# Kernel optimization log

Measured on AMD Instinct MI355X. Metric: run time of the kernel, lower is better.

The kernel has to match this reference:

```python
import jax, jax.numpy as jnp
import numpy as np

N = 50000  # nodes
E = 1600000  # edges
L = 2  # layers
D = 128  # input/hidden dim


def setup_inputs() -> dict:
    key = jax.random.key(0)
    ks = jax.random.split(key, 8)
    s = 1.0 / np.sqrt(D)
    return {
        "x": jax.random.normal(ks[0], (N, D), jnp.float32),
        "edge_index": jax.random.randint(ks[1], (2, E), 0, N, jnp.int64),
        "h": jax.random.normal(ks[2], (L, N, D), jnp.float32),
        "Wx": jax.random.normal(ks[3], (L, 3, D, D), jnp.float32) * s,
        "bx": jax.random.normal(ks[4], (L, 3, D), jnp.float32) * 0.01,
        "Wh": jax.random.normal(ks[5], (L, 3, D, D), jnp.float32) * s,
        "bh": jax.random.normal(ks[6], (L, 3, D), jnp.float32) * 0.01,
    }


def _gcn(x, W, b, src, dst, dinv):
    # GCNConv with added self-loops and symmetric normalization:
    # out = D^{-1/2} (A + I) D^{-1/2} X W + b
    hw = x @ W                                   # [N, H]
    norm = dinv[src] * dinv[dst]                 # [E]
    msg = hw[src] * norm[:, None]                # [E, H]
    agg = jax.ops.segment_sum(msg, dst, num_segments=N)
    agg = agg + hw * (dinv * dinv)[:, None]      # self-loop contribution
    return agg + b


def reference(x, edge_index, h, Wx, bx, Wh, bh):
    src = edge_index[0]
    dst = edge_index[1]
    # in-degree on destination nodes, including self-loop (+1)
    deg = jax.ops.segment_sum(jnp.ones((E,), x.dtype), dst, num_segments=N) + 1.0
    dinv = jax.lax.rsqrt(deg)

    outs = []
    inp = x
    for l in range(L):
        hl = h[l]
        z = jax.nn.sigmoid(_gcn(inp, Wx[l, 0], bx[l, 0], src, dst, dinv)
                           + _gcn(hl, Wh[l, 0], bh[l, 0], src, dst, dinv))
        r = jax.nn.sigmoid(_gcn(inp, Wx[l, 1], bx[l, 1], src, dst, dinv)
                           + _gcn(hl, Wh[l, 1], bh[l, 1], src, dst, dinv))
        h_tilde = jnp.tanh(_gcn(inp, Wx[l, 2], bx[l, 2], src, dst, dinv)
                           + _gcn(r * hl, Wh[l, 2], bh[l, 2], src, dst, dinv))
        out = z * hl + (1.0 - z) * h_tilde
        outs.append(out)
        inp = out
    return jnp.stack(outs, axis=0)  # [L, N, H]
```

## Files before the change

kernel.cpp:

```cpp
#include <hip/hip_runtime.h>

typedef __attribute__((ext_vector_type(8))) unsigned short us8;
typedef __attribute__((ext_vector_type(8))) short s8;
typedef __attribute__((ext_vector_type(4))) float f4;
typedef __attribute__((ext_vector_type(2))) float f2;

#define DEV static __device__ __forceinline__
#define CAP 128
#define NRG 128
#define NBB 256
#define SEGC 128

DEV float bf2f(unsigned short h){ return __uint_as_float(((unsigned)h)<<16); }
DEV unsigned short f2bf(float f){
  unsigned x = __float_as_uint(f);
  x += 0x7fffu + ((x>>16)&1u);
  return (unsigned short)(x>>16);
}
DEV float sigm(float x){ return 1.f/(1.f + __expf(-x)); }

__global__ __launch_bounds__(256) void k_bucket(const int* __restrict__ src,
    const int* __restrict__ dst, unsigned* __restrict__ buf,
    int* __restrict__ cnt2, int e, int n){
  __shared__ int lcnt[NRG];
  int b = blockIdx.x;
  for(int i=threadIdx.x;i<NRG;i+=256) lcnt[i] = 0;
  __syncthreads();
  int chunk = (e + NBB - 1)/NBB;
  int lo = b*chunk;
  int hi = lo + chunk; if(hi>e) hi=e;
  for(int i = lo + threadIdx.x; i < hi; i += 256){
    int d = dst[i], s = src[i];
    int r = (d*NRG)/n;
    int pos = atomicAdd(&lcnt[r], 1);
    if(pos < SEGC)
      buf[((size_t)r*NBB + b)*SEGC + pos] = ((unsigned)d<<16) | (unsigned)s;
  }
  __syncthreads();
  for(int i=threadIdx.x;i<NRG;i+=256) cnt2[i*NBB + b] = lcnt[i];
}

__global__ __launch_bounds__(256) void k_build2(const unsigned* __restrict__ buf,
    const int* __restrict__ cnt2, int* __restrict__ cnt,
    unsigned short* __restrict__ col, int n){
  int r = blockIdx.x;
  int lo = (r*n + NRG-1)/NRG;
  int hi = ((r+1)*n + NRG-1)/NRG;
  int span = hi - lo;
  __shared__ int lc[512];
  for(int i=threadIdx.x; i<span; i+=256) lc[i] = 0;
  __syncthreads();
  int lane = threadIdx.x & 63;
  for(int seg = threadIdx.x>>6; seg < NBB; seg += 4){
    int c = cnt2[r*NBB + seg]; if(c > SEGC) c = SEGC;
    const unsigned* p = buf + ((size_t)r*NBB + seg)*SEGC;
    for(int i = lane; i < c; i += 64){
      unsigned v = p[i];
      int d = (int)(v >> 16), s = (int)(v & 0xffffu);
      int slot = atomicAdd(&lc[d - lo], 1);
      col[(size_t)d*CAP + slot] = (unsigned short)s;
    }
  }
  __syncthreads();
  for(int i=threadIdx.x; i<span; i+=256) cnt[lo + i] = lc[i];
}

__global__ void k_setup(const int* __restrict__ cnt, float* __restrict__ dinv, int n,
                        const float* __restrict__ Wx, const float* __restrict__ Wh,
                        unsigned short* __restrict__ WT){
  int gN = (n + 255)/256;
  int b = blockIdx.x;
  if(b < gN){
    int i = b*256 + threadIdx.x;
    if(i<n) dinv[i] = rsqrtf((float)cnt[i] + 1.0f);
  } else {
    int i = (b-gN)*256 + threadIdx.x;
    int m = i >> 15;
    int rem = i & 32767;
    int j = rem >> 8;
    int k = rem & 255;
    float v = (k<128) ? Wx[((size_t)m*128 + k)*128 + j]
                      : Wh[((size_t)m*128 + (k-128))*128 + j];
    WT[(size_t)m*32768 + j*256 + k] = f2bf(v);
  }
}

__global__ void k_scale2(const float* __restrict__ inp, const float* __restrict__ hl,
                         const float* __restrict__ dinv, unsigned char* __restrict__ y2, int n){
  int i = blockIdx.x*blockDim.x+threadIdx.x;
  if(i >= n*32) return;
  int node = i>>5, d0 = (i&31)*4;
  float dv = dinv[node];
  f4 a = *(const f4*)(inp + (size_t)node*128 + d0);
  f4 b = *(const f4*)(hl  + (size_t)node*128 + d0);
  unsigned pa = __builtin_amdgcn_cvt_pk_fp8_f32(dv*a[0], dv*a[1], 0, false);
  pa = __builtin_amdgcn_cvt_pk_fp8_f32(dv*a[2], dv*a[3], pa, true);
  unsigned pb = __builtin_amdgcn_cvt_pk_fp8_f32(dv*b[0], dv*b[1], 0, false);
  pb = __builtin_amdgcn_cvt_pk_fp8_f32(dv*b[2], dv*b[3], pb, true);
  *(unsigned*)(y2 + (size_t)node*256 + d0)       = pa;
  *(unsigned*)(y2 + (size_t)node*256 + 128 + d0) = pb;
}

template<int DB>
__global__ __launch_bounds__(256) void k_agg(const unsigned char* __restrict__ y,
    const int* __restrict__ cnt, const unsigned short* __restrict__ col,
    const float* __restrict__ dinv, unsigned short* __restrict__ out0, int n)
{
  constexpr int GL = DB/16;
  constexpr int NG = 64/GL;
  constexpr int U = 8;
  int tid = threadIdx.x;
  int wave = tid>>6, lane = tid&63;
  int g = lane/GL, gl = lane%GL;
  int node = blockIdx.x*(4*NG) + wave*NG + g;
  if(node >= n) return;
  const unsigned char* yb = y + (size_t)gl*16;
  float acc[16];
  {
    uint4 q = *(const uint4*)(yb + (size_t)node*DB);
    const unsigned* qw = (const unsigned*)&q;
    #pragma unroll
    for(int w=0;w<4;++w){
      f2 lo = __builtin_amdgcn_cvt_pk_f32_fp8(qw[w], false);
      f2 hi = __builtin_amdgcn_cvt_pk_f32_fp8(qw[w], true);
      acc[w*4+0]=lo[0]; acc[w*4+1]=lo[1]; acc[w*4+2]=hi[0]; acc[w*4+3]=hi[1];
    }
  }
  const unsigned short* myrow = col + (size_t)node*CAP;
  int c_ = cnt[node];
  int last = c_ - 1;
  for(int i=0; i<c_; i += U){
    int s[U];
    #pragma unroll
    for(int u=0;u<U;++u){
      int ii = i + u; ii = (ii < last) ? ii : last;
      s[u] = myrow[ii];
    }
    uint4 v[U];
    #pragma unroll
    for(int u=0;u<U;++u) v[u] = *(const uint4*)(yb + (size_t)s[u]*DB);
    #pragma unroll
    for(int u=0;u<U;++u){
      if(i + u < c_){
        const unsigned* qw = (const unsigned*)&v[u];
        #pragma unroll
        for(int w=0;w<4;++w){
          f2 lo = __builtin_amdgcn_cvt_pk_f32_fp8(qw[w], false);
          f2 hi = __builtin_amdgcn_cvt_pk_f32_fp8(qw[w], true);
          acc[w*4+0]+=lo[0]; acc[w*4+1]+=lo[1]; acc[w*4+2]+=hi[0]; acc[w*4+3]+=hi[1];
        }
      }
    }
  }
  float dv = dinv[node];
  us8 w0, w1;
  #pragma unroll
  for(int j=0;j<8;++j){ w0[j]=f2bf(acc[j]*dv); w1[j]=f2bf(acc[8+j]*dv); }
  int c = gl*16;
  *(us8*)(out0 + (size_t)node*DB + c)     = w0;
  *(us8*)(out0 + (size_t)node*DB + c + 8) = w1;
}

template<int KB>
DEV void stageB512(unsigned char* Bs, const unsigned short* Bsrc, int srcStride,
                   int srcOff, int t){
  constexpr int CPR = KB/8;
  #pragma unroll
  for(int i=0;i<128*CPR/512;++i){
    int c = t + i*512;
    int j = c / CPR, kc = c % CPR;
    us8 v = *(const us8*)(Bsrc + (size_t)j*srcStride + srcOff + kc*8);
    *(us8*)(Bs + ((j*(KB*2) + kc*16) ^ ((j&7)<<4))) = v;
  }
}
template<int NK>
DEV void loadA(const unsigned short* A, int astride, int arow, int nrows, int hi,
               s8 (&a)[NK]){
  const unsigned short* Ap = A + (size_t)(arow < nrows ? arow : 0)*astride + hi*8;
  #pragma unroll
  for(int kk=0;kk<NK;++kk) a[kk] = *(const s8*)(Ap + kk*32);
  if(arow >= nrows){
    #pragma unroll
    for(int kk=0;kk<NK;++kk) a[kk] = (s8)(short)0;
  }
}
template<int KB, int NK, int NA>
DEV void mfmaR(const unsigned char* Bs, const s8 (&a)[NA], int lo, int hi,
               f4 (&acc)[8]){
  static_assert(NK <= NA, "not enough A fragments");
  #pragma unroll
  for(int kk=0;kk<NK;++kk){
    #pragma unroll
    for(int n=0;n<8;++n){
      int j = n*16+lo;
      s8 b = *(const s8*)(Bs + ((j*(KB*2) + kk*64 + hi*16) ^ ((lo&7)<<4)));
      acc[n] = __builtin_amdgcn_mfma_f32_16x16x32_bf16(a[kk], b, acc[n], 0,0,0);
    }
  }
}

__global__ __launch_bounds__(512) void k_gemmRH(
    const unsigned short* __restrict__ axah, const unsigned short* __restrict__ Wr,
    const unsigned short* __restrict__ Wh2, const float* __restrict__ hl,
    const float* __restrict__ dinv, const float* __restrict__ bxr,
    const float* __restrict__ bhr, unsigned char* __restrict__ yq,
    unsigned short* __restrict__ Zbh, int nrows)
{
  __shared__ unsigned char Bs[65536];
  const int t = threadIdx.x, lane = t & 63, lo = lane & 15, hi = lane >> 4;
  const int r0 = blockIdx.x*128 + (t>>6)*16;
  const int arow = r0 + lo;
  s8 a256[8];
  loadA<8>(axah, 256, arow, nrows, hi, a256);
  stageB512<256>(Bs, Wr, 256, 0, t);
  f4 acc[8];
  #pragma unroll
  for(int n=0;n<8;++n) acc[n]=(f4)0.f;
  __syncthreads();
  mfmaR<256,8,8>(Bs, a256, lo, hi, acc);
  #pragma unroll
  for(int n=0;n<8;++n){
    const int colv = n*16 + lo;
    float bz = bxr[colv] + bhr[colv];
    #pragma unroll
    for(int tt=0;tt<4;++tt){
      int row = r0 + hi*4 + tt;
      if(row < nrows){
        float r = sigm(acc[n][tt] + bz);
        float q = dinv[row] * r * hl[(size_t)row*128 + colv];
        unsigned pk = __builtin_amdgcn_cvt_pk_fp8_f32(q, q, 0, false);
        yq[(size_t)row*128 + colv] = (unsigned char)(pk & 0xff);
      }
    }
  }
  __syncthreads();
  stageB512<128>(Bs, Wh2, 256, 0, t);
  __syncthreads();
  #pragma unroll
  for(int n=0;n<8;++n) acc[n]=(f4)0.f;
  mfmaR<128,4,8>(Bs, a256, lo, hi, acc);
  #pragma unroll
  for(int n=0;n<8;++n){
    const int colv = n*16 + lo;
    #pragma unroll
    for(int tt=0;tt<4;++tt){
      int row = r0 + hi*4 + tt;
      if(row < nrows) Zbh[(size_t)row*128 + colv] = f2bf(acc[n][tt]);
    }
  }
}

__global__ __launch_bounds__(512) void k_gemmZF(
    const unsigned short* __restrict__ axah, const unsigned short* __restrict__ aq,
    const unsigned short* __restrict__ Wz, const unsigned short* __restrict__ Wh2,
    const unsigned short* __restrict__ Zbh, const float* __restrict__ hl,
    const float* __restrict__ hnext, const float* __restrict__ dinv,
    const float* __restrict__ bxz, const float* __restrict__ bhz,
    const float* __restrict__ bxh, const float* __restrict__ bhh,
    float* __restrict__ outp, unsigned char* __restrict__ y2out, int nrows)
{
  __shared__ unsigned char Bs[65536];
  const int t = threadIdx.x, lane = t & 63, lo = lane & 15, hi = lane >> 4;
  const int r0 = blockIdx.x*128 + (t>>6)*16;
  const int arow = r0 + lo;
  s8 a256[8], a128[4];
  loadA<8>(axah, 256, arow, nrows, hi, a256);
  loadA<4>(aq, 128, arow, nrows, hi, a128);
  stageB512<256>(Bs, Wz, 256, 0, t);
  f4 accZ[8], accH[8];
  #pragma unroll
  for(int n=0;n<8;++n){ accZ[n]=(f4)0.f; accH[n]=(f4)0.f; }
  __syncthreads();
  mfmaR<256,8,8>(Bs, a256, lo, hi, accZ);
  __syncthreads();
  stageB512<128>(Bs, Wh2, 256, 128, t);
  __syncthreads();
  mfmaR<128,4,4>(Bs, a128, lo, hi, accH);
  #pragma unroll
  for(int n=0;n<8;++n){
    const int colv = n*16 + lo;
    float bz = bxz[colv] + bhz[colv];
    float bh = bxh[colv] + bhh[colv];
    #pragma unroll
    for(int tt=0;tt<4;++tt){
      int row = r0 + hi*4 + tt;
      if(row >= nrows) continue;
      float z  = sigm(accZ[n][tt] + bz);
      float ht = tanhf(accH[n][tt] + bf2f(Zbh[(size_t)row*128 + colv]) + bh);
      float ov = z*hl[(size_t)row*128 + colv] + (1.f - z)*ht;
      outp[(size_t)row*128 + colv] = ov;
      if(y2out){
        float dv = dinv[row];
        unsigned pk = __builtin_amdgcn_cvt_pk_fp8_f32(dv*ov, dv*ov, 0, false);
        y2out[(size_t)row*256 + colv] = (unsigned char)(pk & 0xff);
        float hv = dv * hnext[(size_t)row*128 + colv];
        unsigned ph = __builtin_amdgcn_cvt_pk_fp8_f32(hv, hv, 0, false);
        y2out[(size_t)row*256 + 128 + colv] = (unsigned char)(ph & 0xff);
      }
    }
  }
}

extern "C" void kernel_launch(void* const* d_in, const int* in_sizes, int n_in,
                              void* d_out, int out_size, void* d_ws, size_t ws_size,
                              hipStream_t stream){
  const float* x  = (const float*)d_in[0];
  const int*   ei = (const int*)d_in[1];
  const float* h  = (const float*)d_in[2];
  const float* Wx = (const float*)d_in[3];
  const float* bx = (const float*)d_in[4];
  const float* Wh = (const float*)d_in[5];
  const float* bh = (const float*)d_in[6];
  float* out = (float*)d_out;

  const int N = in_sizes[0] / 128;
  const int E = in_sizes[1] / 2;
  const int L = in_sizes[2] / in_sizes[0];
  const int* src = ei;
  const int* dst = ei + E;

  char* w = (char*)d_ws;
  auto alloc = [&](size_t b)->char*{ char* p = w; w += (b + 255) & ~(size_t)255; return p; };
  int* cnt = (int*)alloc((size_t)N*sizeof(int));
  unsigned short* col = (unsigned short*)alloc((size_t)N*CAP*sizeof(short));
  float* dinv = (float*)alloc((size_t)N*sizeof(float));
  unsigned short* WT = (unsigned short*)alloc((size_t)6*32768*sizeof(short));
  unsigned char* y2 = (unsigned char*)alloc((size_t)N*256);
  unsigned short* axah = (unsigned short*)alloc((size_t)N*256*sizeof(short));
  unsigned char* yq = (unsigned char*)alloc((size_t)N*128);
  unsigned short* aq = (unsigned short*)alloc((size_t)N*128*sizeof(short));
  unsigned short* Zbh = (unsigned short*)alloc((size_t)N*128*sizeof(short));
  unsigned* ebuf = (unsigned*)alloc((size_t)NRG*NBB*SEGC*sizeof(unsigned));
  int* cnt2 = (int*)alloc((size_t)NRG*NBB*sizeof(int));

  const int gN = (N + 255)/256;
  const int gew = (N*32 + 255)/256;
  const int g128 = (N + 127)/128;
  const int gagg4 = (N + 15)/16;
  const int gagg2 = (N + 31)/32;

  k_bucket<<<NBB,256,0,stream>>>(src, dst, ebuf, cnt2, E, N);
  k_build2<<<NRG,256,0,stream>>>(ebuf, cnt2, cnt, col, N);
  k_setup<<<gN + 768,256,0,stream>>>(cnt, dinv, N, Wx, Wh, WT);

  for(int l=0; l<L; ++l){
    const float* hl  = h + (size_t)l*N*128;
    const float* bxz = bx + (size_t)(l*3+0)*128; const float* bhz = bh + (size_t)(l*3+0)*128;
    const float* bxr = bx + (size_t)(l*3+1)*128; const float* bhr = bh + (size_t)(l*3+1)*128;
    const float* bxh = bx + (size_t)(l*3+2)*128; const float* bhh = bh + (size_t)(l*3+2)*128;
    const unsigned short* Wz = WT + (size_t)(l*3+0)*32768;
    const unsigned short* Wr = WT + (size_t)(l*3+1)*32768;
    const unsigned short* Wh2= WT + (size_t)(l*3+2)*32768;

    if(l==0) k_scale2<<<gew,256,0,stream>>>(x, hl, dinv, y2, N);
    k_agg<256><<<gagg4,256,0,stream>>>(y2, cnt, col, dinv, axah, N);
    k_gemmRH<<<g128,512,0,stream>>>(axah, Wr, Wh2, hl, dinv, bxr, bhr, yq, Zbh, N);
    k_agg<128><<<gagg2,256,0,stream>>>(yq, cnt, col, dinv, aq, N);
    k_gemmZF<<<g128,512,0,stream>>>(axah, aq, Wz, Wh2, Zbh, hl,
        (l+1<L) ? (h + (size_t)(l+1)*N*128) : nullptr, dinv,
        bxz, bhz, bxh, bhh, out + (size_t)l*N*128,
        (l+1<L) ? y2 : nullptr, N);
  }
}
```

Measured before the change: 370.6 us.

## Pre-convert hidden state to bf16 and widen gemmZF to 1024 threads

Converts all h layers to bf16 once inside the setup kernel and reads the bf16 copy in scale, gemmRH and gemmZF instead of fp32. gemmZF is restructured to 1024 threads, with both weight tiles staged into separate LDS buffers up front and each wave pair splitting the output columns, removing intermediate barriers. The extra conversion pass adds traffic and lowers the precision of h used in the gating blend.

```diff
diff --git a/kernel.cpp b/kernel.cpp
--- a/kernel.cpp
+++ b/kernel.cpp
@@ -1,6 +1,7 @@
 #include <hip/hip_runtime.h>
 
 typedef __attribute__((ext_vector_type(8))) unsigned short us8;
+typedef __attribute__((ext_vector_type(4))) unsigned short us4;
 typedef __attribute__((ext_vector_type(8))) short s8;
 typedef __attribute__((ext_vector_type(4))) float f4;
 typedef __attribute__((ext_vector_type(2))) float f2;
@@ -67,13 +68,15 @@
 
 __global__ void k_setup(const int* __restrict__ cnt, float* __restrict__ dinv, int n,
                         const float* __restrict__ Wx, const float* __restrict__ Wh,
-                        unsigned short* __restrict__ WT){
+                        unsigned short* __restrict__ WT,
+                        const float* __restrict__ h, unsigned short* __restrict__ hb,
+                        int htotal){
   int gN = (n + 255)/256;
   int b = blockIdx.x;
   if(b < gN){
     int i = b*256 + threadIdx.x;
     if(i<n) dinv[i] = rsqrtf((float)cnt[i] + 1.0f);
-  } else {
+  } else if(b < gN + 768){
     int i = (b-gN)*256 + threadIdx.x;
     int m = i >> 15;
     int rem = i & 32767;
@@ -82,21 +85,30 @@
     float v = (k<128) ? Wx[((size_t)m*128 + k)*128 + j]
                       : Wh[((size_t)m*128 + (k-128))*128 + j];
     WT[(size_t)m*32768 + j*256 + k] = f2bf(v);
-  }
-}
-
-__global__ void k_scale2(const float* __restrict__ inp, const float* __restrict__ hl,
+  } else {
+    size_t i = ((size_t)(b - gN - 768)*256 + threadIdx.x)*4;
+    if(i < (size_t)htotal){
+      f4 v = *(const f4*)(h + i);
+      us4 w;
+      #pragma unroll
+      for(int j=0;j<4;++j) w[j] = f2bf(v[j]);
+      *(us4*)(hb + i) = w;
+    }
+  }
+}
+
+__global__ void k_scale2(const float* __restrict__ inp, const unsigned short* __restrict__ hb0,
                          const float* __restrict__ dinv, unsigned char* __restrict__ y2, int n){
   int i = blockIdx.x*blockDim.x+threadIdx.x;
   if(i >= n*32) return;
   int node = i>>5, d0 = (i&31)*4;
   float dv = dinv[node];
   f4 a = *(const f4*)(inp + (size_t)node*128 + d0);
-  f4 b = *(const f4*)(hl  + (size_t)node*128 + d0);
+  us4 hv = *(const us4*)(hb0 + (size_t)node*128 + d0);
   unsigned pa = __builtin_amdgcn_cvt_pk_fp8_f32(dv*a[0], dv*a[1], 0, false);
   pa = __builtin_amdgcn_cvt_pk_fp8_f32(dv*a[2], dv*a[3], pa, true);
-  unsigned pb = __builtin_amdgcn_cvt_pk_fp8_f32(dv*b[0], dv*b[1], 0, false);
-  pb = __builtin_amdgcn_cvt_pk_fp8_f32(dv*b[2], dv*b[3], pb, true);
+  unsigned pb = __builtin_amdgcn_cvt_pk_fp8_f32(dv*bf2f(hv[0]), dv*bf2f(hv[1]), 0, false);
+  pb = __builtin_amdgcn_cvt_pk_fp8_f32(dv*bf2f(hv[2]), dv*bf2f(hv[3]), pb, true);
   *(unsigned*)(y2 + (size_t)node*256 + d0)       = pa;
   *(unsigned*)(y2 + (size_t)node*256 + 128 + d0) = pb;
 }
@@ -162,14 +174,13 @@
 }
 
 template<int KB>
-DEV void stageB512(unsigned char* Bs, const unsigned short* Bsrc, int srcStride,
-                   int srcOff, int t){
+DEV void stageB512(unsigned char* Bs, const unsigned short* Bsrc, int srcOff, int t){
   constexpr int CPR = KB/8;
   #pragma unroll
   for(int i=0;i<128*CPR/512;++i){
     int c = t + i*512;
     int j = c / CPR, kc = c % CPR;
-    us8 v = *(const us8*)(Bsrc + (size_t)j*srcStride + srcOff + kc*8);
+    us8 v = *(const us8*)(Bsrc + (size_t)j*256 + srcOff + kc*8);
     *(us8*)(Bs + ((j*(KB*2) + kc*16) ^ ((j&7)<<4))) = v;
   }
 }
@@ -201,7 +212,7 @@
 
 __global__ __launch_bounds__(512) void k_gemmRH(
     const unsigned short* __restrict__ axah, const unsigned short* __restrict__ Wr,
-    const unsigned short* __restrict__ Wh2, const float* __restrict__ hl,
+    const unsigned short* __restrict__ Wh2, const unsigned short* __restrict__ hbl,
     const float* __restrict__ dinv, const float* __restrict__ bxr,
     const float* __restrict__ bhr, unsigned char* __restrict__ yq,
     unsigned short* __restrict__ Zbh, int nrows)
@@ -212,7 +223,7 @@
   const int arow = r0 + lo;
   s8 a256[8];
   loadA<8>(axah, 256, arow, nrows, hi, a256);
-  stageB512<256>(Bs, Wr, 256, 0, t);
+  stageB512<256>(Bs, Wr, 0, t);
   f4 acc[8];
   #pragma unroll
   for(int n=0;n<8;++n) acc[n]=(f4)0.f;
@@ -227,14 +238,14 @@
       int row = r0 + hi*4 + tt;
       if(row < nrows){
         float r = sigm(acc[n][tt] + bz);
-        float q = dinv[row] * r * hl[(size_t)row*128 + colv];
+        float q = dinv[row] * r * bf2f(hbl[(size_t)row*128 + colv]);
         unsigned pk = __builtin_amdgcn_cvt_pk_fp8_f32(q, q, 0, false);
         yq[(size_t)row*128 + colv] = (unsigned char)(pk & 0xff);
       }
     }
   }
   __syncthreads();
-  stageB512<128>(Bs, Wh2, 256, 0, t);
+  stageB512<128>(Bs, Wh2, 0, t);
   __syncthreads();
   #pragma unroll
   for(int n=0;n<8;++n) acc[n]=(f4)0.f;
@@ -250,35 +261,80 @@
   }
 }
 
-__global__ __launch_bounds__(512) void k_gemmZF(
+DEV void stageB1k(unsigned char* Bs1, const unsigned short* W, int t){
+  #pragma unroll
+  for(int i=0;i<4;++i){
+    int c = t + i*1024;
+    int j = c >> 5, kc = c & 31;
+    us8 v = *(const us8*)(W + (size_t)j*256 + kc*8);
+    *(us8*)(Bs1 + ((j*512 + kc*16) ^ ((j&7)<<4))) = v;
+  }
+}
+DEV void stageB2k(unsigned char* Bs2, const unsigned short* W, int srcOff, int t){
+  #pragma unroll
+  for(int i=0;i<2;++i){
+    int c = t + i*1024;
+    int j = c >> 4, kc = c & 15;
+    us8 v = *(const us8*)(W + (size_t)j*256 + srcOff + kc*8);
+    *(us8*)(Bs2 + ((j*256 + kc*16) ^ ((j&7)<<4))) = v;
+  }
+}
+DEV void loadA4(const unsigned short* A, int astride, int arow, int nrows, int hi,
+                int koff, s8 (&a)[4]){
+  const unsigned short* Ap = A + (size_t)(arow < nrows ? arow : 0)*astride + koff + hi*8;
+  #pragma unroll
+  for(int kk=0;kk<4;++kk) a[kk] = *(const s8*)(Ap + kk*32);
+  if(arow >= nrows){
+    #pragma unroll
+    for(int kk=0;kk<4;++kk) a[kk] = (s8)(short)0;
+  }
+}
+template<int KROW>
+DEV void mfma4(const unsigned char* Bs, const s8 (&a)[4], int kk0, int jbase,
+               int lo, int hi, f4 (&acc)[4]){
+  #pragma unroll
+  for(int kk=0;kk<4;++kk){
+    #pragma unroll
+    for(int n=0;n<4;++n){
+      int j = jbase + n*16 + lo;
+      s8 b = *(const s8*)(Bs + ((j*KROW + (kk0+kk)*64 + hi*16) ^ ((lo&7)<<4)));
+      acc[n] = __builtin_amdgcn_mfma_f32_16x16x32_bf16(a[kk], b, acc[n], 0,0,0);
+    }
+  }
+}
+
+__global__ __launch_bounds__(1024) void k_gemmZF(
     const unsigned short* __restrict__ axah, const unsigned short* __restrict__ aq,
     const unsigned short* __restrict__ Wz, const unsigned short* __restrict__ Wh2,
-    const unsigned short* __restrict__ Zbh, const float* __restrict__ hl,
-    const float* __restrict__ hnext, const float* __restrict__ dinv,
+    const unsigned short* __restrict__ Zbh, const unsigned short* __restrict__ hbl,
+    const unsigned short* __restrict__ hbn, const float* __restrict__ dinv,
     const float* __restrict__ bxz, const float* __restrict__ bhz,
     const float* __restrict__ bxh, const float* __restrict__ bhh,
     float* __restrict__ outp, unsigned char* __restrict__ y2out, int nrows)
 {
-  __shared__ unsigned char Bs[65536];
+  __shared__ unsigned char Bs1[65536];
+  __shared__ unsigned char Bs2[32768];
   const int t = threadIdx.x, lane = t & 63, lo = lane & 15, hi = lane >> 4;
-  const int r0 = blockIdx.x*128 + (t>>6)*16;
+  const int wid = t >> 6, wrow = wid >> 1, whalf = wid & 1;
+  const int jbase = whalf*64;
+  const int r0 = blockIdx.x*128 + wrow*16;
   const int arow = r0 + lo;
-  s8 a256[8], a128[4];
-  loadA<8>(axah, 256, arow, nrows, hi, a256);
-  loadA<4>(aq, 128, arow, nrows, hi, a128);
-  stageB512<256>(Bs, Wz, 256, 0, t);
-  f4 accZ[8], accH[8];
-  #pragma unroll
-  for(int n=0;n<8;++n){ accZ[n]=(f4)0.f; accH[n]=(f4)0.f; }
-  __syncthreads();
-  mfmaR<256,8,8>(Bs, a256, lo, hi, accZ);
-  __syncthreads();
-  stageB512<128>(Bs, Wh2, 256, 128, t);
-  __syncthreads();
-  mfmaR<128,4,4>(Bs, a128, lo, hi, accH);
-  #pragma unroll
-  for(int n=0;n<8;++n){
-    const int colv = n*16 + lo;
+  stageB1k(Bs1, Wz, t);
+  stageB2k(Bs2, Wh2, 128, t);
+  s8 a03[4], a47[4], aq4[4];
+  loadA4(axah, 256, arow, nrows, hi, 0, a03);
+  loadA4(axah, 256, arow, nrows, hi, 128, a47);
+  loadA4(aq, 128, arow, nrows, hi, 0, aq4);
+  f4 accZ[4], accH[4];
+  #pragma unroll
+  for(int n=0;n<4;++n){ accZ[n]=(f4)0.f; accH[n]=(f4)0.f; }
+  __syncthreads();
+  mfma4<512>(Bs1, a03, 0, jbase, lo, hi, accZ);
+  mfma4<512>(Bs1, a47, 4, jbase, lo, hi, accZ);
+  mfma4<256>(Bs2, aq4, 0, jbase, lo, hi, accH);
+  #pragma unroll
+  for(int n=0;n<4;++n){
+    const int colv = jbase + n*16 + lo;
     float bz = bxz[colv] + bhz[colv];
     float bh = bxh[colv] + bhh[colv];
     #pragma unroll
@@ -287,13 +343,13 @@
       if(row >= nrows) continue;
       float z  = sigm(accZ[n][tt] + bz);
       float ht = tanhf(accH[n][tt] + bf2f(Zbh[(size_t)row*128 + colv]) + bh);
-      float ov = z*hl[(size_t)row*128 + colv] + (1.f - z)*ht;
+      float ov = z*bf2f(hbl[(size_t)row*128 + colv]) + (1.f - z)*ht;
       outp[(size_t)row*128 + colv] = ov;
       if(y2out){
         float dv = dinv[row];
         unsigned pk = __builtin_amdgcn_cvt_pk_fp8_f32(dv*ov, dv*ov, 0, false);
         y2out[(size_t)row*256 + colv] = (unsigned char)(pk & 0xff);
-        float hv = dv * hnext[(size_t)row*128 + colv];
+        float hv = dv * bf2f(hbn[(size_t)row*128 + colv]);
         unsigned ph = __builtin_amdgcn_cvt_pk_fp8_f32(hv, hv, 0, false);
         y2out[(size_t)row*256 + 128 + colv] = (unsigned char)(ph & 0xff);
       }
@@ -325,6 +381,7 @@
   unsigned short* col = (unsigned short*)alloc((size_t)N*CAP*sizeof(short));
   float* dinv = (float*)alloc((size_t)N*sizeof(float));
   unsigned short* WT = (unsigned short*)alloc((size_t)6*32768*sizeof(short));
+  unsigned short* hb = (unsigned short*)alloc((size_t)L*N*128*sizeof(short));
   unsigned char* y2 = (unsigned char*)alloc((size_t)N*256);
   unsigned short* axah = (unsigned short*)alloc((size_t)N*256*sizeof(short));
   unsigned char* yq = (unsigned char*)alloc((size_t)N*128);
@@ -338,13 +395,15 @@
   const int g128 = (N + 127)/128;
   const int gagg4 = (N + 15)/16;
   const int gagg2 = (N + 31)/32;
+  const int htotal = L*N*128;
+  const int ghb = (htotal + 1023)/1024;
 
   k_bucket<<<NBB,256,0,stream>>>(src, dst, ebuf, cnt2, E, N);
   k_build2<<<NRG,256,0,stream>>>(ebuf, cnt2, cnt, col, N);
-  k_setup<<<gN + 768,256,0,stream>>>(cnt, dinv, N, Wx, Wh, WT);
+  k_setup<<<gN + 768 + ghb,256,0,stream>>>(cnt, dinv, N, Wx, Wh, WT, h, hb, htotal);
 
   for(int l=0; l<L; ++l){
-    const float* hl  = h + (size_t)l*N*128;
+    const unsigned short* hbl = hb + (size_t)l*N*128;
     const float* bxz = bx + (size_t)(l*3+0)*128; const float* bhz = bh + (size_t)(l*3+0)*128;
     const float* bxr = bx + (size_t)(l*3+1)*128; const float* bhr = bh + (size_t)(l*3+1)*128;
     const float* bxh = bx + (size_t)(l*3+2)*128; const float* bhh = bh + (size_t)(l*3+2)*128;
@@ -352,12 +411,12 @@
     const unsigned short* Wr = WT + (size_t)(l*3+1)*32768;
     const unsigned short* Wh2= WT + (size_t)(l*3+2)*32768;
 
-    if(l==0) k_scale2<<<gew,256,0,stream>>>(x, hl, dinv, y2, N);
+    if(l==0) k_scale2<<<gew,256,0,stream>>>(x, hbl, dinv, y2, N);
     k_agg<256><<<gagg4,256,0,stream>>>(y2, cnt, col, dinv, axah, N);
-    k_gemmRH<<<g128,512,0,stream>>>(axah, Wr, Wh2, hl, dinv, bxr, bhr, yq, Zbh, N);
+    k_gemmRH<<<g128,512,0,stream>>>(axah, Wr, Wh2, hbl, dinv, bxr, bhr, yq, Zbh, N);
     k_agg<128><<<gagg2,256,0,stream>>>(yq, cnt, col, dinv, aq, N);
-    k_gemmZF<<<g128,512,0,stream>>>(axah, aq, Wz, Wh2, Zbh, hl,
-        (l+1<L) ? (h + (size_t)(l+1)*N*128) : nullptr, dinv,
+    k_gemmZF<<<g128,1024,0,stream>>>(axah, aq, Wz, Wh2, Zbh, hbl,
+        (l+1<L) ? (hb + (size_t)(l+1)*N*128) : nullptr, dinv,
         bxz, bhz, bxh, bhh, out + (size_t)l*N*128,
         (l+1<L) ? y2 : nullptr, N);
   }
```

New measurement: 399.9 us. 1.08x slower.

## Swap MFMA operands for row-contiguous epilogue stores and pre-convert h to bf16

Applied to the files above, without the earlier changes.

The GEMM kernels now put the weights in the MFMA A slot and node features in the B slot, so each lane owns one node and four consecutive output columns. This turns the scattered byte- and short-wide epilogue stores into vectorized 4-element stores and loads. Separately, h is converted once to bf16 in the setup kernel, halving the bytes read from h in later kernels. The cost is an extra pass over all of h in setup, and using bf16 h in the output blend instead of fp32 lowers precision.

```diff
diff --git a/kernel.cpp b/kernel.cpp
--- a/kernel.cpp
+++ b/kernel.cpp
@@ -1,6 +1,7 @@
 #include <hip/hip_runtime.h>
 
 typedef __attribute__((ext_vector_type(8))) unsigned short us8;
+typedef __attribute__((ext_vector_type(4))) unsigned short us4;
 typedef __attribute__((ext_vector_type(8))) short s8;
 typedef __attribute__((ext_vector_type(4))) float f4;
 typedef __attribute__((ext_vector_type(2))) float f2;
@@ -67,13 +68,15 @@
 
 __global__ void k_setup(const int* __restrict__ cnt, float* __restrict__ dinv, int n,
                         const float* __restrict__ Wx, const float* __restrict__ Wh,
-                        unsigned short* __restrict__ WT){
+                        unsigned short* __restrict__ WT,
+                        const float* __restrict__ h, unsigned short* __restrict__ hb,
+                        int htotal){
   int gN = (n + 255)/256;
   int b = blockIdx.x;
   if(b < gN){
     int i = b*256 + threadIdx.x;
     if(i<n) dinv[i] = rsqrtf((float)cnt[i] + 1.0f);
-  } else {
+  } else if(b < gN + 768){
     int i = (b-gN)*256 + threadIdx.x;
     int m = i >> 15;
     int rem = i & 32767;
@@ -82,21 +85,30 @@
     float v = (k<128) ? Wx[((size_t)m*128 + k)*128 + j]
                       : Wh[((size_t)m*128 + (k-128))*128 + j];
     WT[(size_t)m*32768 + j*256 + k] = f2bf(v);
-  }
-}
-
-__global__ void k_scale2(const float* __restrict__ inp, const float* __restrict__ hl,
+  } else {
+    size_t i = ((size_t)(b - gN - 768)*256 + threadIdx.x)*4;
+    if(i < (size_t)htotal){
+      f4 v = *(const f4*)(h + i);
+      us4 w;
+      #pragma unroll
+      for(int j=0;j<4;++j) w[j] = f2bf(v[j]);
+      *(us4*)(hb + i) = w;
+    }
+  }
+}
+
+__global__ void k_scale2(const float* __restrict__ inp, const unsigned short* __restrict__ hb0,
                          const float* __restrict__ dinv, unsigned char* __restrict__ y2, int n){
   int i = blockIdx.x*blockDim.x+threadIdx.x;
   if(i >= n*32) return;
   int node = i>>5, d0 = (i&31)*4;
   float dv = dinv[node];
   f4 a = *(const f4*)(inp + (size_t)node*128 + d0);
-  f4 b = *(const f4*)(hl  + (size_t)node*128 + d0);
+  us4 hv = *(const us4*)(hb0 + (size_t)node*128 + d0);
   unsigned pa = __builtin_amdgcn_cvt_pk_fp8_f32(dv*a[0], dv*a[1], 0, false);
   pa = __builtin_amdgcn_cvt_pk_fp8_f32(dv*a[2], dv*a[3], pa, true);
-  unsigned pb = __builtin_amdgcn_cvt_pk_fp8_f32(dv*b[0], dv*b[1], 0, false);
-  pb = __builtin_amdgcn_cvt_pk_fp8_f32(dv*b[2], dv*b[3], pb, true);
+  unsigned pb = __builtin_amdgcn_cvt_pk_fp8_f32(dv*bf2f(hv[0]), dv*bf2f(hv[1]), 0, false);
+  pb = __builtin_amdgcn_cvt_pk_fp8_f32(dv*bf2f(hv[2]), dv*bf2f(hv[3]), pb, true);
   *(unsigned*)(y2 + (size_t)node*256 + d0)       = pa;
   *(unsigned*)(y2 + (size_t)node*256 + 128 + d0) = pb;
 }
@@ -162,90 +174,91 @@
 }
 
 template<int KB>
-DEV void stageB512(unsigned char* Bs, const unsigned short* Bsrc, int srcStride,
-                   int srcOff, int t){
+DEV void stageB512(unsigned char* Bs, const unsigned short* Bsrc, int srcOff, int t){
   constexpr int CPR = KB/8;
   #pragma unroll
   for(int i=0;i<128*CPR/512;++i){
     int c = t + i*512;
     int j = c / CPR, kc = c % CPR;
-    us8 v = *(const us8*)(Bsrc + (size_t)j*srcStride + srcOff + kc*8);
+    us8 v = *(const us8*)(Bsrc + (size_t)j*256 + srcOff + kc*8);
     *(us8*)(Bs + ((j*(KB*2) + kc*16) ^ ((j&7)<<4))) = v;
   }
 }
 template<int NK>
-DEV void loadA(const unsigned short* A, int astride, int arow, int nrows, int hi,
-               s8 (&a)[NK]){
-  const unsigned short* Ap = A + (size_t)(arow < nrows ? arow : 0)*astride + hi*8;
-  #pragma unroll
-  for(int kk=0;kk<NK;++kk) a[kk] = *(const s8*)(Ap + kk*32);
-  if(arow >= nrows){
-    #pragma unroll
-    for(int kk=0;kk<NK;++kk) a[kk] = (s8)(short)0;
-  }
+DEV void loadB(const unsigned short* A, int astride, int node, int nrows, int hi,
+               s8 (&b)[NK]){
+  const unsigned short* Ap = A + (size_t)(node < nrows ? node : 0)*astride + hi*8;
+  #pragma unroll
+  for(int kk=0;kk<NK;++kk) b[kk] = *(const s8*)(Ap + kk*32);
 }
 template<int KB, int NK, int NA>
-DEV void mfmaR(const unsigned char* Bs, const s8 (&a)[NA], int lo, int hi,
+DEV void mfmaW(const unsigned char* Bs, const s8 (&b)[NA], int lo, int hi,
                f4 (&acc)[8]){
-  static_assert(NK <= NA, "not enough A fragments");
+  static_assert(NK <= NA, "not enough B fragments");
   #pragma unroll
   for(int kk=0;kk<NK;++kk){
     #pragma unroll
     for(int n=0;n<8;++n){
       int j = n*16+lo;
-      s8 b = *(const s8*)(Bs + ((j*(KB*2) + kk*64 + hi*16) ^ ((lo&7)<<4)));
-      acc[n] = __builtin_amdgcn_mfma_f32_16x16x32_bf16(a[kk], b, acc[n], 0,0,0);
+      s8 a = *(const s8*)(Bs + ((j*(KB*2) + kk*64 + hi*16) ^ ((lo&7)<<4)));
+      acc[n] = __builtin_amdgcn_mfma_f32_16x16x32_bf16(a, b[kk], acc[n], 0,0,0);
     }
   }
 }
 
 __global__ __launch_bounds__(512) void k_gemmRH(
     const unsigned short* __restrict__ axah, const unsigned short* __restrict__ Wr,
-    const unsigned short* __restrict__ Wh2, const float* __restrict__ hl,
+    const unsigned short* __restrict__ Wh2, const unsigned short* __restrict__ hbl,
     const float* __restrict__ dinv, const float* __restrict__ bxr,
     const float* __restrict__ bhr, unsigned char* __restrict__ yq,
     unsigned short* __restrict__ Zbh, int nrows)
 {
   __shared__ unsigned char Bs[65536];
   const int t = threadIdx.x, lane = t & 63, lo = lane & 15, hi = lane >> 4;
-  const int r0 = blockIdx.x*128 + (t>>6)*16;
-  const int arow = r0 + lo;
-  s8 a256[8];
-  loadA<8>(axah, 256, arow, nrows, hi, a256);
-  stageB512<256>(Bs, Wr, 256, 0, t);
+  const int node = blockIdx.x*128 + (t>>6)*16 + lo;
+  const bool ok = node < nrows;
+  s8 b256[8];
+  loadB<8>(axah, 256, node, nrows, hi, b256);
+  stageB512<256>(Bs, Wr, 0, t);
   f4 acc[8];
   #pragma unroll
   for(int n=0;n<8;++n) acc[n]=(f4)0.f;
   __syncthreads();
-  mfmaR<256,8,8>(Bs, a256, lo, hi, acc);
-  #pragma unroll
-  for(int n=0;n<8;++n){
-    const int colv = n*16 + lo;
-    float bz = bxr[colv] + bhr[colv];
-    #pragma unroll
-    for(int tt=0;tt<4;++tt){
-      int row = r0 + hi*4 + tt;
-      if(row < nrows){
-        float r = sigm(acc[n][tt] + bz);
-        float q = dinv[row] * r * hl[(size_t)row*128 + colv];
-        unsigned pk = __builtin_amdgcn_cvt_pk_fp8_f32(q, q, 0, false);
-        yq[(size_t)row*128 + colv] = (unsigned char)(pk & 0xff);
-      }
-    }
-  }
-  __syncthreads();
-  stageB512<128>(Bs, Wh2, 256, 0, t);
-  __syncthreads();
-  #pragma unroll
-  for(int n=0;n<8;++n) acc[n]=(f4)0.f;
-  mfmaR<128,4,8>(Bs, a256, lo, hi, acc);
-  #pragma unroll
-  for(int n=0;n<8;++n){
-    const int colv = n*16 + lo;
-    #pragma unroll
-    for(int tt=0;tt<4;++tt){
-      int row = r0 + hi*4 + tt;
-      if(row < nrows) Zbh[(size_t)row*128 + colv] = f2bf(acc[n][tt]);
+  mfmaW<256,8,8>(Bs, b256, lo, hi, acc);
+  if(ok){
+    float dv = dinv[node];
+    const size_t base = (size_t)node*128;
+    #pragma unroll
+    for(int n=0;n<8;++n){
+      int j0 = n*16 + hi*4;
+      f4 b1v = *(const f4*)(bxr + j0);
+      f4 b2v = *(const f4*)(bhr + j0);
+      us4 hv = *(const us4*)(hbl + base + j0);
+      float q0 = dv * sigm(acc[n][0] + b1v[0] + b2v[0]) * bf2f(hv[0]);
+      float q1 = dv * sigm(acc[n][1] + b1v[1] + b2v[1]) * bf2f(hv[1]);
+      float q2 = dv * sigm(acc[n][2] + b1v[2] + b2v[2]) * bf2f(hv[2]);
+      float q3 = dv * sigm(acc[n][3] + b1v[3] + b2v[3]) * bf2f(hv[3]);
+      unsigned pk = __builtin_amdgcn_cvt_pk_fp8_f32(q0, q1, 0, false);
+      pk = __builtin_amdgcn_cvt_pk_fp8_f32(q2, q3, pk, true);
+      *(unsigned*)(yq + base + j0) = pk;
+    }
+  }
+  __syncthreads();
+  stageB512<128>(Bs, Wh2, 0, t);
+  f4 accH[8];
+  #pragma unroll
+  for(int n=0;n<8;++n) accH[n]=(f4)0.f;
+  __syncthreads();
+  mfmaW<128,4,8>(Bs, b256, lo, hi, accH);
+  if(ok){
+    const size_t base = (size_t)node*128;
+    #pragma unroll
+    for(int n=0;n<8;++n){
+      int j0 = n*16 + hi*4;
+      us4 w;
+      #pragma unroll
+      for(int tt=0;tt<4;++tt) w[tt] = f2bf(accH[n][tt]);
+      *(us4*)(Zbh + base + j0) = w;
     }
   }
 }
@@ -253,49 +266,60 @@
 __global__ __launch_bounds__(512) void k_gemmZF(
     const unsigned short* __restrict__ axah, const unsigned short* __restrict__ aq,
     const unsigned short* __restrict__ Wz, const unsigned short* __restrict__ Wh2,
-    const unsigned short* __restrict__ Zbh, const float* __restrict__ hl,
-    const float* __restrict__ hnext, const float* __restrict__ dinv,
+    const unsigned short* __restrict__ Zbh, const unsigned short* __restrict__ hbl,
+    const unsigned short* __restrict__ hbn, const float* __restrict__ dinv,
     const float* __restrict__ bxz, const float* __restrict__ bhz,
     const float* __restrict__ bxh, const float* __restrict__ bhh,
     float* __restrict__ outp, unsigned char* __restrict__ y2out, int nrows)
 {
   __shared__ unsigned char Bs[65536];
   const int t = threadIdx.x, lane = t & 63, lo = lane & 15, hi = lane >> 4;
-  const int r0 = blockIdx.x*128 + (t>>6)*16;
-  const int arow = r0 + lo;
-  s8 a256[8], a128[4];
-  loadA<8>(axah, 256, arow, nrows, hi, a256);
-  loadA<4>(aq, 128, arow, nrows, hi, a128);
-  stageB512<256>(Bs, Wz, 256, 0, t);
-  f4 accZ[8], accH[8];
-  #pragma unroll
-  for(int n=0;n<8;++n){ accZ[n]=(f4)0.f; accH[n]=(f4)0.f; }
-  __syncthreads();
-  mfmaR<256,8,8>(Bs, a256, lo, hi, accZ);
-  __syncthreads();
-  stageB512<128>(Bs, Wh2, 256, 128, t);
-  __syncthreads();
-  mfmaR<128,4,4>(Bs, a128, lo, hi, accH);
-  #pragma unroll
-  for(int n=0;n<8;++n){
-    const int colv = n*16 + lo;
-    float bz = bxz[colv] + bhz[colv];
-    float bh = bxh[colv] + bhh[colv];
-    #pragma unroll
-    for(int tt=0;tt<4;++tt){
-      int row = r0 + hi*4 + tt;
-      if(row >= nrows) continue;
-      float z  = sigm(accZ[n][tt] + bz);
-      float ht = tanhf(accH[n][tt] + bf2f(Zbh[(size_t)row*128 + colv]) + bh);
-      float ov = z*hl[(size_t)row*128 + colv] + (1.f - z)*ht;
-      outp[(size_t)row*128 + colv] = ov;
+  const int node = blockIdx.x*128 + (t>>6)*16 + lo;
+  const bool ok = node < nrows;
+  s8 b256[8], bq[4];
+  loadB<8>(axah, 256, node, nrows, hi, b256);
+  loadB<4>(aq, 128, node, nrows, hi, bq);
+  stageB512<256>(Bs, Wz, 0, t);
+  f4 accZ[8];
+  #pragma unroll
+  for(int n=0;n<8;++n) accZ[n]=(f4)0.f;
+  __syncthreads();
+  mfmaW<256,8,8>(Bs, b256, lo, hi, accZ);
+  __syncthreads();
+  stageB512<128>(Bs, Wh2, 128, t);
+  f4 accH[8];
+  #pragma unroll
+  for(int n=0;n<8;++n) accH[n]=(f4)0.f;
+  __syncthreads();
+  mfmaW<128,4,4>(Bs, bq, lo, hi, accH);
+  if(ok){
+    float dv = dinv[node];
+    const size_t base = (size_t)node*128;
+    #pragma unroll
+    for(int n=0;n<8;++n){
+      int j0 = n*16 + hi*4;
+      f4 bz1 = *(const f4*)(bxz + j0);
+      f4 bz2 = *(const f4*)(bhz + j0);
+      f4 bh1 = *(const f4*)(bxh + j0);
+      f4 bh2 = *(const f4*)(bhh + j0);
+      us4 zb = *(const us4*)(Zbh + base + j0);
+      us4 hv = *(const us4*)(hbl + base + j0);
+      f4 o;
+      #pragma unroll
+      for(int tt=0;tt<4;++tt){
+        float z  = sigm(accZ[n][tt] + bz1[tt] + bz2[tt]);
+        float ht = tanhf(accH[n][tt] + bf2f(zb[tt]) + bh1[tt] + bh2[tt]);
+        o[tt] = z*bf2f(hv[tt]) + (1.f - z)*ht;
+      }
+      *(f4*)(outp + base + j0) = o;
       if(y2out){
-        float dv = dinv[row];
-        unsigned pk = __builtin_amdgcn_cvt_pk_fp8_f32(dv*ov, dv*ov, 0, false);
-        y2out[(size_t)row*256 + colv] = (unsigned char)(pk & 0xff);
-        float hv = dv * hnext[(size_t)row*128 + colv];
-        unsigned ph = __builtin_amdgcn_cvt_pk_fp8_f32(hv, hv, 0, false);
-        y2out[(size_t)row*256 + 128 + colv] = (unsigned char)(ph & 0xff);
+        unsigned pk = __builtin_amdgcn_cvt_pk_fp8_f32(dv*o[0], dv*o[1], 0, false);
+        pk = __builtin_amdgcn_cvt_pk_fp8_f32(dv*o[2], dv*o[3], pk, true);
+        *(unsigned*)(y2out + (size_t)node*256 + j0) = pk;
+        us4 hn = *(const us4*)(hbn + base + j0);
+        unsigned ph = __builtin_amdgcn_cvt_pk_fp8_f32(dv*bf2f(hn[0]), dv*bf2f(hn[1]), 0, false);
+        ph = __builtin_amdgcn_cvt_pk_fp8_f32(dv*bf2f(hn[2]), dv*bf2f(hn[3]), ph, true);
+        *(unsigned*)(y2out + (size_t)node*256 + 128 + j0) = ph;
       }
     }
   }
@@ -325,6 +349,7 @@
   unsigned short* col = (unsigned short*)alloc((size_t)N*CAP*sizeof(short));
   float* dinv = (float*)alloc((size_t)N*sizeof(float));
   unsigned short* WT = (unsigned short*)alloc((size_t)6*32768*sizeof(short));
+  unsigned short* hb = (unsigned short*)alloc((size_t)L*N*128*sizeof(short));
   unsigned char* y2 = (unsigned char*)alloc((size_t)N*256);
   unsigned short* axah = (unsigned short*)alloc((size_t)N*256*sizeof(short));
   unsigned char* yq = (unsigned char*)alloc((size_t)N*128);
@@ -338,13 +363,15 @@
   const int g128 = (N + 127)/128;
   const int gagg4 = (N + 15)/16;
   const int gagg2 = (N + 31)/32;
+  const int htotal = L*N*128;
+  const int ghb = (htotal + 1023)/1024;
 
   k_bucket<<<NBB,256,0,stream>>>(src, dst, ebuf, cnt2, E, N);
   k_build2<<<NRG,256,0,stream>>>(ebuf, cnt2, cnt, col, N);
-  k_setup<<<gN + 768,256,0,stream>>>(cnt, dinv, N, Wx, Wh, WT);
+  k_setup<<<gN + 768 + ghb,256,0,stream>>>(cnt, dinv, N, Wx, Wh, WT, h, hb, htotal);
 
   for(int l=0; l<L; ++l){
-    const float* hl  = h + (size_t)l*N*128;
+    const unsigned short* hbl = hb + (size_t)l*N*128;
     const float* bxz = bx + (size_t)(l*3+0)*128; const float* bhz = bh + (size_t)(l*3+0)*128;
     const float* bxr = bx + (size_t)(l*3+1)*128; const float* bhr = bh + (size_t)(l*3+1)*128;
     const float* bxh = bx + (size_t)(l*3+2)*128; const float* bhh = bh + (size_t)(l*3+2)*128;
@@ -352,12 +379,12 @@
     const unsigned short* Wr = WT + (size_t)(l*3+1)*32768;
     const unsigned short* Wh2= WT + (size_t)(l*3+2)*32768;
 
-    if(l==0) k_scale2<<<gew,256,0,stream>>>(x, hl, dinv, y2, N);
+    if(l==0) k_scale2<<<gew,256,0,stream>>>(x, hbl, dinv, y2, N);
     k_agg<256><<<gagg4,256,0,stream>>>(y2, cnt, col, dinv, axah, N);
-    k_gemmRH<<<g128,512,0,stream>>>(axah, Wr, Wh2, hl, dinv, bxr, bhr, yq, Zbh, N);
+    k_gemmRH<<<g128,512,0,stream>>>(axah, Wr, Wh2, hbl, dinv, bxr, bhr, yq, Zbh, N);
     k_agg<128><<<gagg2,256,0,stream>>>(yq, cnt, col, dinv, aq, N);
-    k_gemmZF<<<g128,512,0,stream>>>(axah, aq, Wz, Wh2, Zbh, hl,
-        (l+1<L) ? (h + (size_t)(l+1)*N*128) : nullptr, dinv,
+    k_gemmZF<<<g128,512,0,stream>>>(axah, aq, Wz, Wh2, Zbh, hbl,
+        (l+1<L) ? (hb + (size_t)(l+1)*N*128) : nullptr, dinv,
         bxz, bhz, bxh, bhh, out + (size_t)l*N*128,
         (l+1<L) ? y2 : nullptr, N);
   }
```

Result: no change. 364.1 us (-1.8%).
